# Kernel optimization log

Measured on AMD Instinct MI355X. Metric: run time of the kernel, lower is better.

Reference implementation:

```python
import jax, jax.numpy as jnp
import numpy as np

EPS = 1e-8

def rms_norm(x, scale):
    # norm(2,-1)/sqrt(d); x / (rms + eps) * scale
    d = x.shape[-1]
    norm = jnp.sqrt(jnp.sum(x * x, axis=-1, keepdims=True))
    rms = norm / jnp.sqrt(jnp.asarray(d, x.dtype))
    return scale * (x / (rms + EPS))

def setup_inputs() -> dict:
    key = jax.random.key(0)
    B, N, C, FF = 2, 2048, 1024, 4096
    ks = jax.random.split(key, 12)
    s = 0.02
    return {
        "x":  jax.random.normal(ks[0], (B, N, C), jnp.float32),
        "wq": jax.random.normal(ks[1], (C, C), jnp.float32) * s,
        "bq": jnp.zeros((C,), jnp.float32),
        "wk": jax.random.normal(ks[2], (C, C), jnp.float32) * s,
        "bk": jnp.zeros((C,), jnp.float32),
        "wv": jax.random.normal(ks[3], (C, C), jnp.float32) * s,
        "bv": jnp.zeros((C,), jnp.float32),
        "wo": jax.random.normal(ks[4], (C, C), jnp.float32) * s,
        "bo": jnp.zeros((C,), jnp.float32),
        "scale1": jnp.ones((C,), jnp.float32),
        "scale2": jnp.ones((C,), jnp.float32),
        "w1": jax.random.normal(ks[5], (C, FF), jnp.float32) * s,
        "b1": jnp.zeros((FF,), jnp.float32),
        "w2": jax.random.normal(ks[6], (FF, C), jnp.float32) * s,
        "b2": jnp.zeros((C,), jnp.float32),
    }

def reference(x, wq, bq, wk, bk, wv, bv, wo, bo, scale1, scale2, w1, b1, w2, b2):
    B, N, C = x.shape
    H = 16
    D = C // H

    residual = x
    xn = rms_norm(x, scale1)

    def heads(y):  # [B,N,C] -> [B,H,N,D]
        return y.reshape(B, N, H, D).transpose(0, 2, 1, 3)

    q = heads(xn @ wq + bq)
    k = heads(xn @ wk + bk)
    v = heads(xn @ wv + bv)

    # apply_rotary_pos_emb with cos=sin=1: q' = q - roll(q,1,-1), same for k
    q = q - jnp.roll(q, 1, axis=-1)
    k = k - jnp.roll(k, 1, axis=-1)

    # explicit attention (no causal mask in original)
    scores = jnp.einsum('bhnd,bhmd->bhnm', q, k) / jnp.sqrt(jnp.asarray(D, x.dtype))
    probs = jax.nn.softmax(scores, axis=-1)
    attn = jnp.einsum('bhnm,bhmd->bhnd', probs, v)
    attn = attn.transpose(0, 2, 1, 3).reshape(B, N, C)
    attn = attn @ wo + bo

    x = residual + attn
    residual = x
    xn = rms_norm(x, scale2)
    h = jax.nn.gelu(xn @ w1 + b1, approximate=False)  # torch GELU default = exact
    ffn_out = h @ w2 + b2
    return residual + ffn_out
```

## Files before the change

kernel.cpp:

```cpp
#include <hip/hip_runtime.h>
#include <hip/hip_bf16.h>
#include <math.h>

typedef unsigned short u16;
typedef short s16x8 __attribute__((ext_vector_type(8)));
typedef __bf16 bf16x8v __attribute__((ext_vector_type(8)));
typedef float f32x4 __attribute__((ext_vector_type(4)));
typedef unsigned short u16x4 __attribute__((ext_vector_type(4)));

struct Ptr4 { float* p[4]; };
struct TW6 {
    const float* w[6]; u16* o[6]; int mode[6];
    const float *bq, *bk, *bv; float* bqkv;
};

__device__ __forceinline__ u16 f2b(float f) {
    __hip_bfloat16 h = __float2bfloat16(f);
    return __builtin_bit_cast(u16, h);
}

__device__ __forceinline__ f32x4 mfma16(s16x8 a, s16x8 b, f32x4 c) {
    return __builtin_amdgcn_mfma_f32_16x16x32_bf16(
        __builtin_bit_cast(bf16x8v, a), __builtin_bit_cast(bf16x8v, b), c, 0, 0, 0);
}

__device__ __forceinline__ void gl_lds16(const void* g, void* l) {
    typedef const unsigned int __attribute__((address_space(1))) * gp_t;
    typedef unsigned int __attribute__((address_space(3))) * lp_t;
    __builtin_amdgcn_global_load_lds((gp_t)(unsigned long long)g,
                                     (lp_t)(unsigned int)(unsigned long long)l,
                                     16, 0, 0);
}

__device__ __forceinline__ float gelu_fast(float v) {
    float u = 1.5957691216f * (v + 0.044715f * v * v * v);
    return v / (1.f + __expf(-u));
}

__global__ __launch_bounds__(256) void prep_weights(TW6 io) {
    const int z = blockIdx.z, bx = blockIdx.x, by = blockIdx.y;
    const float* W; u16* Wt; int mode = 0, N_, K_, n0, k0;
    if (z < 4) {
        if (bx >= 32) {
            if (z == 0 && bx < 44 && by == 0) {
                const int i = (bx - 32) * 256 + threadIdx.x;
                const int d = i & 1023;
                const int dp = (d & ~63) | ((d + 63) & 63);
                float v;
                if (i < 1024) v = 0.125f * (io.bq[d] - io.bq[dp]);
                else if (i < 2048) v = io.bk[d] - io.bk[dp];
                else v = io.bv[d];
                io.bqkv[i] = v;
            }
            return;
        }
        W = io.w[z]; Wt = io.o[z]; mode = io.mode[z];
        N_ = 1024; K_ = 1024; n0 = bx * 32; k0 = by * 32;
    } else if (z == 4) {
        W = io.w[4]; Wt = io.o[4]; N_ = 4096; K_ = 1024; n0 = bx * 32; k0 = by * 32;
    } else {
        W = io.w[5]; Wt = io.o[5]; N_ = 1024; K_ = 4096; n0 = by * 32; k0 = bx * 32;
    }
    __shared__ u16 tile[32][33];
    const int tx = threadIdx.x & 31, ty = threadIdx.x >> 5;
    const int n = n0 + tx;
    const int np = (n & ~63) | ((n + 63) & 63);
    const float s = (mode == 1) ? 0.125f : 1.f;
#pragma unroll
    for (int i = 0; i < 32; i += 8) {
        const size_t r = (size_t)(k0 + ty + i) * N_;
        float v = W[r + n];
        if (mode) v = (v - W[r + np]) * s;
        tile[ty + i][tx] = f2b(v);
    }
    __syncthreads();
#pragma unroll
    for (int i = 0; i < 32; i += 8)
        Wt[(size_t)(n0 + ty + i) * K_ + k0 + tx] = tile[tx][ty + i];
}

__global__ __launch_bounds__(256) void transpose_v(const u16* __restrict__ qkv,
                                                   u16* __restrict__ vT) {
    __shared__ u16 tile[32][33];
    const int tx = threadIdx.x & 31, ty = threadIdx.x >> 5;
    const int n0 = blockIdx.x * 32, d0 = blockIdx.y * 32, bh = blockIdx.z;
    const int b = bh >> 4, h = bh & 15;
#pragma unroll
    for (int i = 0; i < 32; i += 8)
        tile[ty + i][tx] =
            qkv[(size_t)(b * 2048 + n0 + ty + i) * 3072 + 2048 + h * 64 + d0 + tx];
    __syncthreads();
#pragma unroll
    for (int i = 0; i < 32; i += 8)
        vT[((size_t)bh * 64 + d0 + ty + i) * 2048 + n0 + tx] = tile[tx][ty + i];
}

__global__ __launch_bounds__(256) void rmsnorm_kernel(const float* __restrict__ x,
                                                      const float* __restrict__ scale,
                                                      u16* __restrict__ out) {
    __shared__ float red[4];
    const int t = threadIdx.x, row = blockIdx.x;
    const float4* xr = (const float4*)(x + (size_t)row * 1024);
    float4 v = xr[t];
    float ss = v.x * v.x + v.y * v.y + v.z * v.z + v.w * v.w;
#pragma unroll
    for (int off = 1; off < 64; off <<= 1) ss += __shfl_xor(ss, off);
    if ((t & 63) == 0) red[t >> 6] = ss;
    __syncthreads();
    float tot = red[0] + red[1] + red[2] + red[3];
    float inv = 1.f / (sqrtf(tot * (1.f / 1024.f)) + 1e-8f);
    const float4* sr = (const float4*)scale;
    float4 s = sr[t];
    u16x4 o;
    o[0] = f2b(v.x * inv * s.x);
    o[1] = f2b(v.y * inv * s.y);
    o[2] = f2b(v.z * inv * s.z);
    o[3] = f2b(v.w * inv * s.w);
    ((u16x4*)(out + (size_t)row * 1024))[t] = o;
}

template <int EPI>
__global__ __launch_bounds__(256) void gemm_kernel(const u16* __restrict__ A,
                                                   const u16* __restrict__ Bt,
                                                   const float* __restrict__ bias,
                                                   const float* __restrict__ resid,
                                                   void* __restrict__ outp,
                                                   int M, int N, int K) {
    __shared__ __align__(16) u16 As[128 * 64];
    __shared__ __align__(16) u16 Bs[128 * 64];
    const int t = threadIdx.x, lane = t & 63;
    const int w = t >> 6, wm = (w >> 1) * 64, wn = (w & 1) * 64;
    const int c = lane & 15, qd = lane >> 4;
    const int n0 = blockIdx.x * 128, m0 = blockIdx.y * 128;

    const int srow = t >> 3;
    const int sch8 = ((t & 7) ^ (srow & 7)) * 8;
    const u16* Ag = A + (size_t)(m0 + srow) * K + sch8;
    const u16* Bg = Bt + (size_t)(n0 + srow) * K + sch8;
    const size_t rstride = (size_t)32 * K;

    f32x4 acc[4][4] = {};
    for (int kt = 0; kt < K; kt += 64) {
        __syncthreads();
#pragma unroll
        for (int g = 0; g < 4; g++) {
            gl_lds16(Ag + g * rstride, &As[t * 8 + g * 2048]);
            gl_lds16(Bg + g * rstride, &Bs[t * 8 + g * 2048]);
        }
        Ag += 64;
        Bg += 64;
        __syncthreads();
#pragma unroll
        for (int s = 0; s < 2; s++) {
            s16x8 a[4], b[4];
#pragma unroll
            for (int im = 0; im < 4; im++)
                a[im] = *(const s16x8*)&As[(wm + im * 16 + c) * 64 +
                                           (((s * 4 + qd) ^ (c & 7)) * 8)];
#pragma unroll
            for (int jn = 0; jn < 4; jn++)
                b[jn] = *(const s16x8*)&Bs[(wn + jn * 16 + c) * 64 +
                                           (((s * 4 + qd) ^ (c & 7)) * 8)];
#pragma unroll
            for (int im = 0; im < 4; im++)
#pragma unroll
                for (int jn = 0; jn < 4; jn++)
                    acc[im][jn] = mfma16(a[im], b[jn], acc[im][jn]);
        }
    }

#pragma unroll
    for (int im = 0; im < 4; im++) {
#pragma unroll
        for (int jn = 0; jn < 4; jn++) {
            const int colg = n0 + wn + jn * 16 + c;
            const float bv = bias[colg];
#pragma unroll
            for (int r = 0; r < 4; r++) {
                const int rowg = m0 + wm + im * 16 + qd * 4 + r;
                const size_t off = (size_t)rowg * N + colg;
                float v = acc[im][jn][r] + bv;
                if (EPI == 0) {
                    ((u16*)outp)[off] = f2b(v);
                } else if (EPI == 1) {
                    ((float*)outp)[off] = v + resid[off];
                } else {
                    ((u16*)outp)[off] = f2b(gelu_fast(v));
                }
            }
        }
    }
}

__global__ __launch_bounds__(256) void gemm_splitk(const u16* __restrict__ A,
                                                   const u16* __restrict__ Bt,
                                                   Ptr4 parts,
                                                   int N, int Ktot, int Kc) {
    __shared__ __align__(16) u16 As[128 * 64];
    __shared__ __align__(16) u16 Bs[128 * 64];
    const int t = threadIdx.x, lane = t & 63;
    const int w = t >> 6, wm = (w >> 1) * 64, wn = (w & 1) * 64;
    const int c = lane & 15, qd = lane >> 4;
    const int n0 = blockIdx.x * 128, m0 = blockIdx.y * 128;
    const int z = blockIdx.z;
    float* out = parts.p[z];

    const int srow = t >> 3;
    const int sch8 = ((t & 7) ^ (srow & 7)) * 8;
    const u16* Ag = A + (size_t)(m0 + srow) * Ktot + z * Kc + sch8;
    const u16* Bg = Bt + (size_t)(n0 + srow) * Ktot + z * Kc + sch8;
    const size_t rstride = (size_t)32 * Ktot;

    f32x4 acc[4][4] = {};
    for (int kt = 0; kt < Kc; kt += 64) {
        __syncthreads();
#pragma unroll
        for (int g = 0; g < 4; g++) {
            gl_lds16(Ag + g * rstride, &As[t * 8 + g * 2048]);
            gl_lds16(Bg + g * rstride, &Bs[t * 8 + g * 2048]);
        }
        Ag += 64;
        Bg += 64;
        __syncthreads();
#pragma unroll
        for (int s = 0; s < 2; s++) {
            s16x8 a[4], b[4];
#pragma unroll
            for (int im = 0; im < 4; im++)
                a[im] = *(const s16x8*)&As[(wm + im * 16 + c) * 64 +
                                           (((s * 4 + qd) ^ (c & 7)) * 8)];
#pragma unroll
            for (int jn = 0; jn < 4; jn++)
                b[jn] = *(const s16x8*)&Bs[(wn + jn * 16 + c) * 64 +
                                           (((s * 4 + qd) ^ (c & 7)) * 8)];
#pragma unroll
            for (int im = 0; im < 4; im++)
#pragma unroll
                for (int jn = 0; jn < 4; jn++)
                    acc[im][jn] = mfma16(a[im], b[jn], acc[im][jn]);
        }
    }

#pragma unroll
    for (int im = 0; im < 4; im++)
#pragma unroll
        for (int jn = 0; jn < 4; jn++) {
            const int colg = n0 + wn + jn * 16 + c;
#pragma unroll
            for (int r = 0; r < 4; r++) {
                const int rowg = m0 + wm + im * 16 + qd * 4 + r;
                out[(size_t)rowg * N + colg] = acc[im][jn][r];
            }
        }
}

template <int S, bool NORM>
__global__ __launch_bounds__(256) void reduce_kernel(Ptr4 parts,
                                                     const float* __restrict__ bias,
                                                     const float* __restrict__ resid,
                                                     const float* __restrict__ scale,
                                                     float* __restrict__ yout,
                                                     u16* __restrict__ xnout) {
    __shared__ float red[4];
    const int t = threadIdx.x, row = blockIdx.x;
    const size_t base = (size_t)row * 1024;
    float4 v = ((const float4*)(resid + base))[t];
    float4 bv = ((const float4*)bias)[t];
    v.x += bv.x; v.y += bv.y; v.z += bv.z; v.w += bv.w;
#pragma unroll
    for (int s = 0; s < S; s++) {
        float4 pv = ((const float4*)(parts.p[s] + base))[t];
        v.x += pv.x; v.y += pv.y; v.z += pv.z; v.w += pv.w;
    }
    ((float4*)(yout + base))[t] = v;
    if (NORM) {
        float ss = v.x * v.x + v.y * v.y + v.z * v.z + v.w * v.w;
#pragma unroll
        for (int off = 1; off < 64; off <<= 1) ss += __shfl_xor(ss, off);
        if ((t & 63) == 0) red[t >> 6] = ss;
        __syncthreads();
        float tot = red[0] + red[1] + red[2] + red[3];
        float inv = 1.f / (sqrtf(tot * (1.f / 1024.f)) + 1e-8f);
        float4 s = ((const float4*)scale)[t];
        u16x4 o;
        o[0] = f2b(v.x * inv * s.x);
        o[1] = f2b(v.y * inv * s.y);
        o[2] = f2b(v.z * inv * s.z);
        o[3] = f2b(v.w * inv * s.w);
        ((u16x4*)(xnout + base))[t] = o;
    }
}

__global__ __launch_bounds__(256, 3) void attn_kernel(const u16* __restrict__ qkv,
                                                      const u16* __restrict__ vT,
                                                      u16* __restrict__ attn) {
    __shared__ __align__(16) u16 Ks[2][64 * 64];
    __shared__ __align__(16) u16 Vs[2][64 * 64];
    __shared__ __align__(16) u16 Ps[4 * 32 * 64];

    const int t = threadIdx.x, lane = t & 63, w = t >> 6;
    const int c = lane & 15, qd = lane >> 4;
    const int bh = blockIdx.y, b = bh >> 4, h = bh & 15;
    const int q0 = blockIdx.x * 128;
    const size_t rowbase = (size_t)b * 2048;

    const u16* kg = qkv + rowbase * 3072 + 1024 + h * 64;
    const u16* vg = vT + (size_t)bh * 64 * 2048;

    const int srow = t >> 3;
    const int sch = (t & 7) ^ (srow & 7);

    const u16* kptr = kg + (size_t)srow * 3072 + sch * 8;
    const u16* vptr = vg + (size_t)srow * 2048 + sch * 8;

    gl_lds16(kptr, &Ks[0][t * 8]);
    gl_lds16(kptr + (size_t)32 * 3072, &Ks[0][2048 + t * 8]);
    gl_lds16(vptr, &Vs[0][t * 8]);
    gl_lds16(vptr + (size_t)32 * 2048, &Vs[0][2048 + t * 8]);

    s16x8 qf[2][2];
    {
        const u16* qg = qkv + (rowbase + q0 + w * 32) * 3072 + h * 64;
#pragma unroll
        for (int im = 0; im < 2; im++)
#pragma unroll
            for (int ks = 0; ks < 2; ks++)
                qf[im][ks] = *(const s16x8*)&qg[(size_t)(im * 16 + c) * 3072 +
                                                ks * 32 + qd * 8];
    }
    __syncthreads();

    float lsum[2][4] = {};
    f32x4 o[2][4] = {};
    u16* Pw = &Ps[w * 32 * 64];

    for (int it = 0; it < 32; it++) {
        const int buf = it & 1;
        const u16* Kb = Ks[buf];
        const u16* Vb = Vs[buf];

        if (it + 1 < 32) {
            u16* Kn = Ks[buf ^ 1];
            u16* Vn = Vs[buf ^ 1];
            const size_t ko = (size_t)(it + 1) * 64 * 3072;
            const size_t vo = (size_t)(it + 1) * 64;
            gl_lds16(kptr + ko, &Kn[t * 8]);
            gl_lds16(kptr + ko + (size_t)32 * 3072, &Kn[2048 + t * 8]);
            gl_lds16(vptr + vo, &Vn[t * 8]);
            gl_lds16(vptr + vo + (size_t)32 * 2048, &Vn[2048 + t * 8]);
        }

        s16x8 kf[2][4], vf[2][4];
#pragma unroll
        for (int ks = 0; ks < 2; ks++)
#pragma unroll
            for (int j = 0; j < 4; j++) {
                const int rrow = j * 16 + c;
                const int sw = ((ks * 4 + qd) ^ (rrow & 7)) * 8;
                kf[ks][j] = *(const s16x8*)&Kb[rrow * 64 + sw];
                vf[ks][j] = *(const s16x8*)&Vb[rrow * 64 + sw];
            }

#pragma unroll
        for (int im = 0; im < 2; im++) {
            f32x4 sc[4] = {};
#pragma unroll
            for (int ks = 0; ks < 2; ks++)
#pragma unroll
                for (int jn = 0; jn < 4; jn++)
                    sc[jn] = mfma16(qf[im][ks], kf[ks][jn], sc[jn]);
#pragma unroll
            for (int r = 0; r < 4; r++) {
                const int prow = im * 16 + qd * 4 + r;
                float s = 0.f;
#pragma unroll
                for (int jn = 0; jn < 4; jn++) {
                    float p = __expf(sc[jn][r]);
                    s += p;
                    Pw[prow * 64 + (((jn * 2 + (c >> 3)) ^ (prow & 7)) * 8) + (c & 7)] =
                        f2b(p);
                }
                lsum[im][r] += s;
            }
        }

#pragma unroll
        for (int im = 0; im < 2; im++)
#pragma unroll
            for (int ks = 0; ks < 2; ks++) {
                s16x8 pf = *(const s16x8*)&Pw[(im * 16 + c) * 64 +
                                              (((ks * 4 + qd) ^ (c & 7)) * 8)];
#pragma unroll
                for (int jd = 0; jd < 4; jd++)
                    o[im][jd] = mfma16(pf, vf[ks][jd], o[im][jd]);
            }
        __syncthreads();
    }

#pragma unroll
    for (int im = 0; im < 2; im++)
#pragma unroll
        for (int r = 0; r < 4; r++)
#pragma unroll
            for (int off2 = 1; off2 < 16; off2 <<= 1)
                lsum[im][r] += __shfl_xor(lsum[im][r], off2);

    const int orow_base = b * 2048 + q0 + w * 32;
#pragma unroll
    for (int im = 0; im < 2; im++)
#pragma unroll
        for (int r = 0; r < 4; r++) {
            const float inv = 1.f / lsum[im][r];
            const int grow = orow_base + im * 16 + qd * 4 + r;
#pragma unroll
            for (int jd = 0; jd < 4; jd++)
                attn[(size_t)grow * 1024 + h * 64 + jd * 16 + c] =
                    f2b(o[im][jd][r] * inv);
        }
}

extern "C" void kernel_launch(void* const* d_in, const int* in_sizes, int n_in,
                              void* d_out, int out_size, void* d_ws, size_t ws_size,
                              hipStream_t stream) {
    const float* x = (const float*)d_in[0];
    const float* wq = (const float*)d_in[1];
    const float* bq = (const float*)d_in[2];
    const float* wk = (const float*)d_in[3];
    const float* bk = (const float*)d_in[4];
    const float* wv = (const float*)d_in[5];
    const float* bv = (const float*)d_in[6];
    const float* wo = (const float*)d_in[7];
    const float* bo = (const float*)d_in[8];
    const float* scale1 = (const float*)d_in[9];
    const float* scale2 = (const float*)d_in[10];
    const float* w1 = (const float*)d_in[11];
    const float* b1 = (const float*)d_in[12];
    const float* w2 = (const float*)d_in[13];
    const float* b2 = (const float*)d_in[14];
    float* out = (float*)d_out;

    char* ws = (char*)d_ws;
    size_t off = 0;
    auto alloc = [&](size_t bytes) -> char* {
        char* p = ws + off;
        off += (bytes + 255) & ~(size_t)255;
        return p;
    };
    u16* wqkvT = (u16*)alloc((size_t)3072 * 1024 * 2);
    u16* woT   = (u16*)alloc((size_t)1024 * 1024 * 2);
    u16* w1T   = (u16*)alloc((size_t)4096 * 1024 * 2);
    u16* w2T   = (u16*)alloc((size_t)1024 * 4096 * 2);
    float* bqkv = (float*)alloc(3072 * 4);
    u16* xn    = (u16*)alloc((size_t)4096 * 1024 * 2);
    u16* qkv   = (u16*)alloc((size_t)4096 * 3072 * 2);
    u16* vT    = (u16*)alloc((size_t)32 * 64 * 2048 * 2);
    u16* attnb = (u16*)alloc((size_t)4096 * 1024 * 2);
    float* y1  = (float*)alloc((size_t)4096 * 1024 * 4);
    u16* hbuf  = (u16*)alloc((size_t)4096 * 4096 * 2);

    const size_t SPLIT = (size_t)4096 * 1024;
    Ptr4 po; po.p[0] = (float*)qkv; po.p[1] = (float*)qkv + SPLIT;
    po.p[2] = nullptr; po.p[3] = nullptr;
    Ptr4 pf; pf.p[0] = (float*)xn; pf.p[1] = (float*)xn + SPLIT;
    pf.p[2] = (float*)xn + 2 * SPLIT; pf.p[3] = (float*)wqkvT;

    dim3 blk(256);

    TW6 tw;
    tw.w[0] = wq; tw.o[0] = wqkvT;                          tw.mode[0] = 1;
    tw.w[1] = wk; tw.o[1] = wqkvT + (size_t)1024 * 1024;    tw.mode[1] = 2;
    tw.w[2] = wv; tw.o[2] = wqkvT + (size_t)2048 * 1024;    tw.mode[2] = 0;
    tw.w[3] = wo; tw.o[3] = woT;                            tw.mode[3] = 0;
    tw.w[4] = w1; tw.o[4] = w1T;                            tw.mode[4] = 0;
    tw.w[5] = w2; tw.o[5] = w2T;                            tw.mode[5] = 0;
    tw.bq = bq; tw.bk = bk; tw.bv = bv; tw.bqkv = bqkv;
    prep_weights<<<dim3(128, 32, 6), blk, 0, stream>>>(tw);

    rmsnorm_kernel<<<4096, blk, 0, stream>>>(x, scale1, xn);
    gemm_kernel<0><<<dim3(24, 32), blk, 0, stream>>>(xn, wqkvT, bqkv, nullptr, qkv, 4096, 3072, 1024);
    transpose_v<<<dim3(64, 2, 32), blk, 0, stream>>>(qkv, vT);
    attn_kernel<<<dim3(16, 32), blk, 0, stream>>>(qkv, vT, attnb);
    gemm_splitk<<<dim3(8, 32, 2), blk, 0, stream>>>(attnb, woT, po, 1024, 1024, 512);
    reduce_kernel<2, true><<<4096, blk, 0, stream>>>(po, bo, x, scale2, y1, xn);
    gemm_kernel<2><<<dim3(32, 32), blk, 0, stream>>>(xn, w1T, b1, nullptr, hbuf, 4096, 4096, 1024);
    gemm_splitk<<<dim3(8, 32, 4), blk, 0, stream>>>(hbuf, w2T, pf, 1024, 4096, 1024);
    reduce_kernel<4, false><<<4096, blk, 0, stream>>>(pf, b2, y1, nullptr, out, nullptr);
}
```

Before: 385.7 us.

## Split attention over key dimension into two partitions with separate reduce kernel

The attention kernel now splits the 2048 keys into two halves via a z grid dimension, doubling the block count from 512 to 1024 so more CUs are filled. Each half writes unnormalized fp32 partial outputs and row sums to scratch buffers (reusing hbuf and y1), and a new reduce kernel combines them and normalizes to bf16. K/V double buffering is replaced by a single buffer with two barriers per iteration, which removes load/compute overlap. The change adds fp32 partial traffic and an extra launch, and relies on scratch-buffer aliasing being safe.

After: 408.3 us. +5.8%, slower.

```diff
diff --git a/kernel.cpp b/kernel.cpp
--- a/kernel.cpp
+++ b/kernel.cpp
@@ -291,17 +291,19 @@
     }
 }
 
-__global__ __launch_bounds__(256, 3) void attn_kernel(const u16* __restrict__ qkv,
-                                                      const u16* __restrict__ vT,
-                                                      u16* __restrict__ attn) {
-    __shared__ __align__(16) u16 Ks[2][64 * 64];
-    __shared__ __align__(16) u16 Vs[2][64 * 64];
+__global__ __launch_bounds__(256) void attn_kernel(const u16* __restrict__ qkv,
+                                                   const u16* __restrict__ vT,
+                                                   float* __restrict__ Opart,
+                                                   float* __restrict__ lpart) {
+    __shared__ __align__(16) u16 Ks[64 * 64];
+    __shared__ __align__(16) u16 Vs[64 * 64];
     __shared__ __align__(16) u16 Ps[4 * 32 * 64];
 
     const int t = threadIdx.x, lane = t & 63, w = t >> 6;
     const int c = lane & 15, qd = lane >> 4;
     const int bh = blockIdx.y, b = bh >> 4, h = bh & 15;
     const int q0 = blockIdx.x * 128;
+    const int z = blockIdx.z;
     const size_t rowbase = (size_t)b * 2048;
 
     const u16* kg = qkv + rowbase * 3072 + 1024 + h * 64;
@@ -310,13 +312,8 @@
     const int srow = t >> 3;
     const int sch = (t & 7) ^ (srow & 7);
 
-    const u16* kptr = kg + (size_t)srow * 3072 + sch * 8;
-    const u16* vptr = vg + (size_t)srow * 2048 + sch * 8;
-
-    gl_lds16(kptr, &Ks[0][t * 8]);
-    gl_lds16(kptr + (size_t)32 * 3072, &Ks[0][2048 + t * 8]);
-    gl_lds16(vptr, &Vs[0][t * 8]);
-    gl_lds16(vptr + (size_t)32 * 2048, &Vs[0][2048 + t * 8]);
+    const u16* kptr = kg + (size_t)(z * 1024 + srow) * 3072 + sch * 8;
+    const u16* vptr = vg + (size_t)srow * 2048 + z * 1024 + sch * 8;
 
     s16x8 qf[2][2];
     {
@@ -328,27 +325,20 @@
                 qf[im][ks] = *(const s16x8*)&qg[(size_t)(im * 16 + c) * 3072 +
                                                 ks * 32 + qd * 8];
     }
-    __syncthreads();
 
     float lsum[2][4] = {};
     f32x4 o[2][4] = {};
     u16* Pw = &Ps[w * 32 * 64];
 
-    for (int it = 0; it < 32; it++) {
-        const int buf = it & 1;
-        const u16* Kb = Ks[buf];
-        const u16* Vb = Vs[buf];
-
-        if (it + 1 < 32) {
-            u16* Kn = Ks[buf ^ 1];
-            u16* Vn = Vs[buf ^ 1];
-            const size_t ko = (size_t)(it + 1) * 64 * 3072;
-            const size_t vo = (size_t)(it + 1) * 64;
-            gl_lds16(kptr + ko, &Kn[t * 8]);
-            gl_lds16(kptr + ko + (size_t)32 * 3072, &Kn[2048 + t * 8]);
-            gl_lds16(vptr + vo, &Vn[t * 8]);
-            gl_lds16(vptr + vo + (size_t)32 * 2048, &Vn[2048 + t * 8]);
-        }
+    for (int it = 0; it < 16; it++) {
+        __syncthreads();
+        gl_lds16(kptr, &Ks[t * 8]);
+        gl_lds16(kptr + (size_t)32 * 3072, &Ks[2048 + t * 8]);
+        gl_lds16(vptr, &Vs[t * 8]);
+        gl_lds16(vptr + (size_t)32 * 2048, &Vs[2048 + t * 8]);
+        kptr += (size_t)64 * 3072;
+        vptr += 64;
+        __syncthreads();
 
         s16x8 kf[2][4], vf[2][4];
 #pragma unroll
@@ -357,8 +347,8 @@
             for (int j = 0; j < 4; j++) {
                 const int rrow = j * 16 + c;
                 const int sw = ((ks * 4 + qd) ^ (rrow & 7)) * 8;
-                kf[ks][j] = *(const s16x8*)&Kb[rrow * 64 + sw];
-                vf[ks][j] = *(const s16x8*)&Vb[rrow * 64 + sw];
+                kf[ks][j] = *(const s16x8*)&Ks[rrow * 64 + sw];
+                vf[ks][j] = *(const s16x8*)&Vs[rrow * 64 + sw];
             }
 
 #pragma unroll
@@ -394,7 +384,6 @@
                 for (int jd = 0; jd < 4; jd++)
                     o[im][jd] = mfma16(pf, vf[ks][jd], o[im][jd]);
             }
-        __syncthreads();
     }
 
 #pragma unroll
@@ -405,18 +394,36 @@
             for (int off2 = 1; off2 < 16; off2 <<= 1)
                 lsum[im][r] += __shfl_xor(lsum[im][r], off2);
 
+    float* Op = Opart + (size_t)z * 4096 * 1024;
     const int orow_base = b * 2048 + q0 + w * 32;
 #pragma unroll
     for (int im = 0; im < 2; im++)
 #pragma unroll
         for (int r = 0; r < 4; r++) {
-            const float inv = 1.f / lsum[im][r];
             const int grow = orow_base + im * 16 + qd * 4 + r;
 #pragma unroll
             for (int jd = 0; jd < 4; jd++)
-                attn[(size_t)grow * 1024 + h * 64 + jd * 16 + c] =
-                    f2b(o[im][jd][r] * inv);
-        }
+                Op[(size_t)grow * 1024 + h * 64 + jd * 16 + c] = o[im][jd][r];
+            if (c == 0) lpart[z * 65536 + grow * 16 + h] = lsum[im][r];
+        }
+}
+
+__global__ __launch_bounds__(256) void attn_reduce(const float* __restrict__ Opart,
+                                                   const float* __restrict__ lpart,
+                                                   u16* __restrict__ attnb) {
+    const int t = threadIdx.x, row = blockIdx.x;
+    const size_t base = (size_t)row * 1024;
+    const int head = t >> 4;
+    const float l = lpart[row * 16 + head] + lpart[65536 + row * 16 + head];
+    const float inv = 1.f / l;
+    float4 a = ((const float4*)(Opart + base))[t];
+    float4 b = ((const float4*)(Opart + (size_t)4096 * 1024 + base))[t];
+    u16x4 o;
+    o[0] = f2b((a.x + b.x) * inv);
+    o[1] = f2b((a.y + b.y) * inv);
+    o[2] = f2b((a.z + b.z) * inv);
+    o[3] = f2b((a.w + b.w) * inv);
+    ((u16x4*)(attnb + base))[t] = o;
 }
 
 extern "C" void kernel_launch(void* const* d_in, const int* in_sizes, int n_in,
@@ -479,7 +486,8 @@
     rmsnorm_kernel<<<4096, blk, 0, stream>>>(x, scale1, xn);
     gemm_kernel<0><<<dim3(24, 32), blk, 0, stream>>>(xn, wqkvT, bqkv, nullptr, qkv, 4096, 3072, 1024);
     transpose_v<<<dim3(64, 2, 32), blk, 0, stream>>>(qkv, vT);
-    attn_kernel<<<dim3(16, 32), blk, 0, stream>>>(qkv, vT, attnb);
+    attn_kernel<<<dim3(16, 32, 2), blk, 0, stream>>>(qkv, vT, (float*)hbuf, y1);
+    attn_reduce<<<4096, blk, 0, stream>>>((float*)hbuf, y1, attnb);
     gemm_splitk<<<dim3(8, 32, 2), blk, 0, stream>>>(attnb, woT, po, 1024, 1024, 512);
     reduce_kernel<2, true><<<4096, blk, 0, stream>>>(po, bo, x, scale2, y1, xn);
     gemm_kernel<2><<<dim3(32, 32), blk, 0, stream>>>(xn, w1T, b1, nullptr, hbuf, 4096, 4096, 1024);
```
